# Performance work log

Measured on AMD Instinct MI355X. Metric: run time of the kernel, lower is better.

The kernel has to match this reference:

```python
import jax, jax.numpy as jnp
import numpy as np

EPS = 1e-5
GROUPS = 4


def _bn(x, g, b, axes):
    # training-mode batch norm (fresh torch module runs in train mode): biased var
    mean = x.mean(axes, keepdims=True)
    var = x.var(axes, keepdims=True)
    sh = (1, -1) + (1,) * (x.ndim - 2)
    return (x - mean) * jax.lax.rsqrt(var + EPS) * g.reshape(sh) + b.reshape(sh)


def _prelu(x, a):
    return jnp.where(x >= 0, x, a * x)


def _avgpool2(x):
    B, C, H, W = x.shape
    return x.reshape(B, C, H // 2, 2, W // 2, 2).mean(axis=(3, 5))


def _axial(x, dim, qkv_w, qkv_g, qkv_b, sim_g, sim_b, rel_emb, out_g, out_b):
    # x: [B, C, H, W]; dim==0 attends over H, dim==1 over W
    if dim == 0:
        x = jnp.transpose(x, (0, 3, 1, 2))  # [B, W, C, H]
    else:
        x = jnp.transpose(x, (0, 2, 1, 3))  # [B, H, C, W]
    B, D1, C, A = x.shape
    x = x.reshape(B * D1, C, A)
    # 1x1 conv1d (no bias) + BN1d
    qkv = jnp.einsum('oc,nca->noa', qkv_w, x)
    qkv = _bn(qkv, qkv_g, qkv_b, axes=(0, 2))
    gc = qkv.shape[1] // GROUPS // 2  # group_channels
    qkv = qkv.reshape(B * D1, GROUPS, 2 * gc, A)
    q = qkv[:, :, : gc // 2]
    k = qkv[:, :, gc // 2: gc]
    v = qkv[:, :, gc:]
    # relative position embeddings gathered into [2*gc, A, A]
    ri = jnp.arange(A)[:, None] - jnp.arange(A)[None, :] + A - 1  # [A, A]
    emb = rel_emb[:, ri]
    qe, ke, ve = emb[: gc // 2], emb[gc // 2: gc], emb[gc:]
    q_emb = jnp.einsum('ngci,cij->ngij', q, qe)
    k_emb = jnp.einsum('ngci,cij->ngij', k, ke)
    qk = jnp.einsum('ngci,ngcj->ngij', q_emb, k_emb)
    sim = jnp.concatenate([qk, q_emb, k_emb], axis=1)  # [N, 3g, A, A]
    sim = _bn(sim, sim_g, sim_b, axes=(0, 2, 3))
    sim = sim.reshape(B * D1, 3, GROUPS, A, A).sum(axis=1)
    sim = jax.nn.softmax(sim, axis=3)
    am = jnp.einsum('ngij,ngcj->ngci', sim, v)
    ame = jnp.einsum('ngij,cij->ngci', sim, ve)
    # cat along last dim then view -> equivalent to stacking pairs on a new axis
    out = jnp.stack([am, ame], axis=3).reshape(B * D1, 2 * GROUPS * gc, A)
    out = _bn(out, out_g, out_b, axes=(0, 2))
    out = out.reshape(B, D1, GROUPS * gc, 2, A).sum(axis=3)
    if dim == 0:
        return jnp.transpose(out, (0, 2, 3, 1))  # [B, C_out, H, W]
    return jnp.transpose(out, (0, 2, 1, 3))


def _cbn(x, g, b, lin_w, latent):
    x = _bn(x, g, b, axes=(0, 2, 3))
    sb = lin_w @ latent  # [2*C]
    C = x.shape[1]
    scale, bias = sb[:C], sb[C:]
    return scale[None, :, None, None] * x + bias[None, :, None, None]


def _forward(input, latent_vector, w_in, cbn1_g, cbn1_b, cbn1_lin, prelu1,
             ax0_qkv_w, ax0_qkv_g, ax0_qkv_b, ax0_sim_g, ax0_sim_b, ax0_rel_emb, ax0_out_g, ax0_out_b,
             ax1_qkv_w, ax1_qkv_g, ax1_qkv_b, ax1_sim_g, ax1_sim_b, ax1_rel_emb, ax1_out_g, ax1_out_b,
             w_out, cbn2_g, cbn2_b, cbn2_lin, prelu2):
    out = jnp.einsum('oc,bchw->bohw', w_in, input)
    out = _prelu(_cbn(out, cbn1_g, cbn1_b, cbn1_lin, latent_vector), prelu1)
    out = _axial(out, 0, ax0_qkv_w, ax0_qkv_g, ax0_qkv_b, ax0_sim_g, ax0_sim_b, ax0_rel_emb, ax0_out_g, ax0_out_b)
    out = _axial(out, 1, ax1_qkv_w, ax1_qkv_g, ax1_qkv_b, ax1_sim_g, ax1_sim_b, ax1_rel_emb, ax1_out_g, ax1_out_b)
    out = _avgpool2(out)
    out = jnp.einsum('oc,bchw->bohw', w_out, out)
    out = _cbn(out, cbn2_g, cbn2_b, cbn2_lin, latent_vector)
    out = out + _avgpool2(input)  # residual_mapping is Identity (in==out channels)
    return _prelu(out, prelu2)


def setup_inputs() -> dict:
    key = jax.random.key(0)
    ks = jax.random.split(key, 12)
    C, L, S = 64, 256, 128
    gc = C // GROUPS  # 16
    d = {}
    d['input'] = jax.random.normal(ks[0], (4, C, S, S), dtype=jnp.float32)
    d['latent_vector'] = jax.random.normal(ks[1], (L,), dtype=jnp.float32)
    d['w_in'] = jax.random.normal(ks[2], (C, C), dtype=jnp.float32) * 0.1
    d['cbn1_g'] = jnp.ones((C,), jnp.float32)
    d['cbn1_b'] = jnp.zeros((C,), jnp.float32)
    d['cbn1_lin'] = jax.random.normal(ks[3], (2 * C, L), dtype=jnp.float32) * 0.05
    d['prelu1'] = jnp.float32(0.25)
    for i, k1, k2 in [(0, ks[4], ks[5]), (1, ks[6], ks[7])]:
        d[f'ax{i}_qkv_w'] = jax.random.normal(k1, (2 * C, C), dtype=jnp.float32) * 0.1
        d[f'ax{i}_qkv_g'] = jnp.ones((2 * C,), jnp.float32)
        d[f'ax{i}_qkv_b'] = jnp.zeros((2 * C,), jnp.float32)
        d[f'ax{i}_sim_g'] = jnp.ones((3 * GROUPS,), jnp.float32)
        d[f'ax{i}_sim_b'] = jnp.zeros((3 * GROUPS,), jnp.float32)
        d[f'ax{i}_rel_emb'] = jax.random.normal(k2, (2 * gc, 2 * S - 1), dtype=jnp.float32)
        d[f'ax{i}_out_g'] = jnp.ones((2 * C,), jnp.float32)
        d[f'ax{i}_out_b'] = jnp.zeros((2 * C,), jnp.float32)
    d['w_out'] = jax.random.normal(ks[8], (C, C), dtype=jnp.float32) * 0.1
    d['cbn2_g'] = jnp.ones((C,), jnp.float32)
    d['cbn2_b'] = jnp.zeros((C,), jnp.float32)
    d['cbn2_lin'] = jax.random.normal(ks[9], (2 * C, L), dtype=jnp.float32) * 0.05
    d['prelu2'] = jnp.float32(0.25)
    return d


def reference(input, latent_vector, w_in, cbn1_g, cbn1_b, cbn1_lin, prelu1,
              ax0_qkv_w, ax0_qkv_g, ax0_qkv_b, ax0_sim_g, ax0_sim_b, ax0_rel_emb, ax0_out_g, ax0_out_b,
              ax1_qkv_w, ax1_qkv_g, ax1_qkv_b, ax1_sim_g, ax1_sim_b, ax1_rel_emb, ax1_out_g, ax1_out_b,
              w_out, cbn2_g, cbn2_b, cbn2_lin, prelu2):
    return _forward(input, latent_vector, w_in, cbn1_g, cbn1_b, cbn1_lin, prelu1,
                    ax0_qkv_w, ax0_qkv_g, ax0_qkv_b, ax0_sim_g, ax0_sim_b, ax0_rel_emb, ax0_out_g, ax0_out_b,
                    ax1_qkv_w, ax1_qkv_g, ax1_qkv_b, ax1_sim_g, ax1_sim_b, ax1_rel_emb, ax1_out_g, ax1_out_b,
                    w_out, cbn2_g, cbn2_b, cbn2_lin, prelu2)
```

## Files before the change

kernel.cpp:

```cpp
#include <hip/hip_runtime.h>

#define EPS 1e-5f
#define SP 16
#define SWA(x) ((((x) >> 2) & 3) << 3)

typedef __attribute__((ext_vector_type(4))) _Float16 h4;
typedef __attribute__((ext_vector_type(8))) _Float16 h8;
typedef __attribute__((ext_vector_type(4))) float f4;
typedef __attribute__((ext_vector_type(4))) unsigned int u4;

#define WS_SB1        0
#define WS_SB2        128
#define WS_STAT_C1    256
#define WS_STAT_QKV0  2304
#define WS_STAT_QKV1  6400
#define WS_STAT_SIM0  10496
#define WS_STAT_SIM1  10880
#define WS_STAT_OUT0  11264
#define WS_STAT_OUT1  15360
#define WS_STAT_C2    19456
#define WS_STAT_END   21504
#define WS_COEFQ0     21504
#define WS_COEFQ1     21760

#define WS_R1  32768
#define WS_R2  (WS_R1 + 8388608)
#define WS_R3  (WS_R2 + 8388608)

#define SIM_CNT_INV (1.f / 1048576.f)

#define L_QEA 0
#define L_KEB 32768
#define L_RET 65536
#define L_AQ  73728
#define L_AK  77824
#define L_V   73728

__device__ __forceinline__ float wred(float v) {
    #pragma unroll
    for (int off = 32; off > 0; off >>= 1) v += __shfl_down(v, off, 64);
    return v;
}

__global__ void k_prep0(const float* __restrict__ lin1, const float* __restrict__ lin2,
                        const float* __restrict__ latent, float* __restrict__ ws) {
    int t = threadIdx.x;
    for (int i = 256 + t; i < WS_STAT_END; i += 256) ws[i] = 0.f;
    const float* lin = (t < 128) ? lin1 : lin2;
    int row = t & 127;
    float s = 0.f;
    for (int l = 0; l < 256; ++l) s += lin[row * 256 + l] * latent[l];
    ws[(t < 128 ? WS_SB1 : WS_SB2) + row] = s;
}

__global__ __launch_bounds__(256) void k_conv1(const float* __restrict__ in,
                                               const float* __restrict__ w,
                                               float* __restrict__ out,
                                               float* __restrict__ stat) {
    __shared__ float ws_[2048];
    __shared__ float sred[2][4][32];
    int t = threadIdx.x;
    int lane = t & 63, wv = t >> 6;
    int oh = blockIdx.x & 1;
    int pb = blockIdx.x >> 1;
    for (int i = t; i < 2048; i += 256) ws_[i] = w[oh * 2048 + i];
    __syncthreads();
    int p  = pb * 256 + t;
    int b  = p >> 14, hw = p & 16383;
    const float* ip = in + b * 64 * 16384 + hw;
    float x[64];
    #pragma unroll
    for (int c = 0; c < 64; ++c) x[c] = ip[c * 16384];
    float* op = out + b * 64 * 16384 + hw + oh * 32 * 16384;
    for (int o2 = 0; o2 < 32; ++o2) {
        float acc = 0.f;
        #pragma unroll
        for (int c = 0; c < 64; ++c) acc += ws_[o2 * 64 + c] * x[c];
        op[o2 * 16384] = acc;
        float s = wred(acc), ss = wred(acc * acc);
        if (lane == 0) { sred[0][wv][o2] = s; sred[1][wv][o2] = ss; }
    }
    __syncthreads();
    if (t < 64) {
        int o2 = t & 31, st = t >> 5;
        float v = sred[st][0][o2] + sred[st][1][o2] + sred[st][2][o2] + sred[st][3][o2];
        atomicAdd(&stat[(st * 64 + oh * 32 + o2) * SP], v);
    }
}

__global__ __launch_bounds__(256) void k_t1t(const float* __restrict__ src, float* __restrict__ dst,
                                             const float* __restrict__ ws,
                                             const float* __restrict__ g1,
                                             const float* __restrict__ b1,
                                             const float* __restrict__ prelu1) {
    __shared__ float tile[32][33];
    int bid = blockIdx.x;
    int wt = bid & 3, ht = (bid >> 2) & 3, c = (bid >> 4) & 63, b = bid >> 10;
    float mean = ws[WS_STAT_C1 + c * SP] * (1.f / 65536.f);
    float var  = ws[WS_STAT_C1 + (64 + c) * SP] * (1.f / 65536.f) - mean * mean;
    float ab = g1[c] * rsqrtf(var + EPS);
    float sc = ws[WS_SB1 + c], bi = ws[WS_SB1 + 64 + c];
    float A = sc * ab;
    float Bb = sc * (b1[c] - mean * ab) + bi;
    float slope = *prelu1;
    int tx = threadIdx.x & 31, ty = threadIdx.x >> 5;
    const float* sp = src + ((b * 64 + c) * 128 + ht * 32) * 128 + wt * 32;
    for (int r = 0; r < 4; ++r) {
        float v = sp[(ty + r * 8) * 128 + tx];
        v = A * v + Bb;
        v = v >= 0.f ? v : slope * v;
        tile[ty + r * 8][tx] = v;
    }
    __syncthreads();
    float* dp = dst + b * 1048576 + (wt * 32) * 8192 + c * 128 + ht * 32;
    for (int r = 0; r < 4; ++r)
        dp[(ty + r * 8) * 8192 + tx] = tile[tx][ty + r * 8];
}

__global__ __launch_bounds__(256) void k_qkvm(const float* __restrict__ x, const float* __restrict__ w,
                                              _Float16* __restrict__ out, float* __restrict__ statq,
                                              int SB, int SR, int SC) {
    __shared__ __align__(16) _Float16 Wh[8192];
    __shared__ __align__(16) _Float16 Xt[8192];
    int t = threadIdx.x;
    int lane = t & 63, wv = t >> 6;
    int l15 = lane & 15, g4 = lane >> 4;
    int n = (blockIdx.x & 7) * 64 + (blockIdx.x >> 3);
    int b = n >> 7, r = n & 127;
    for (int i = t; i < 8192; i += 256) {
        int o = i >> 6, c = i & 63;
        Wh[o * 64 + (c ^ ((o & 7) << 3))] = (_Float16)w[i];
    }
    const float* xp = x + b * SB + r * SR;
    for (int i = t; i < 8192; i += 256) {
        int c = i >> 7, a = i & 127;
        Xt[a * 64 + (c ^ ((a & 7) << 3))] = (_Float16)xp[c * SC + a];
    }
    __syncthreads();
    _Float16* op = out + n * 16384;
    float sA[2][4] = {{0.f,0.f,0.f,0.f},{0.f,0.f,0.f,0.f}};
    float qA[2][4] = {{0.f,0.f,0.f,0.f},{0.f,0.f,0.f,0.f}};
    #pragma unroll
    for (int ot2 = 0; ot2 < 2; ++ot2) {
        int orow = (wv * 2 + ot2) * 16 + l15;
        h8 af[2];
        #pragma unroll
        for (int kk = 0; kk < 2; ++kk)
            af[kk] = *(const h8*)&Wh[orow * 64 + ((kk * 32 + g4 * 8) ^ ((orow & 7) << 3))];
        #pragma unroll
        for (int at = 0; at < 8; ++at) {
            int arow = at * 16 + l15;
            f4 c4 = {0.f, 0.f, 0.f, 0.f};
            #pragma unroll
            for (int kk = 0; kk < 2; ++kk) {
                h8 bf = *(const h8*)&Xt[arow * 64 + ((kk * 32 + g4 * 8) ^ ((arow & 7) << 3))];
                c4 = __builtin_amdgcn_mfma_f32_16x16x32_f16(af[kk], bf, c4, 0, 0, 0);
            }
            #pragma unroll
            for (int r4 = 0; r4 < 4; ++r4) {
                int o = (wv * 2 + ot2) * 16 + g4 * 4 + r4;
                float v = c4[r4];
                op[o * 128 + at * 16 + l15] = (_Float16)v;
                sA[ot2][r4] += v; qA[ot2][r4] += v * v;
            }
        }
    }
    #pragma unroll
    for (int ot2 = 0; ot2 < 2; ++ot2)
        #pragma unroll
        for (int r4 = 0; r4 < 4; ++r4) {
            float s = sA[ot2][r4], ss = qA[ot2][r4];
            #pragma unroll
            for (int msk = 1; msk < 16; msk <<= 1) {
                s += __shfl_xor(s, msk, 64); ss += __shfl_xor(ss, msk, 64);
            }
            if (l15 == 0) {
                int o = (wv * 2 + ot2) * 16 + g4 * 4 + r4;
                atomicAdd(&statq[o * SP], s);
                atomicAdd(&statq[(128 + o) * SP], ss);
            }
        }
}

__global__ void k_coefq(const float* __restrict__ statq, const float* __restrict__ qg,
                        const float* __restrict__ qb, float* __restrict__ cq) {
    int c = threadIdx.x; if (c >= 128) return;
    float mean = statq[c * SP] * (1.f / 65536.f);
    float var  = statq[(128 + c) * SP] * (1.f / 65536.f) - mean * mean;
    float A = qg[c] * rsqrtf(var + EPS);
    cq[c] = A;
    cq[128 + c] = qb[c] - mean * A;
}

__device__ __forceinline__ void stage_aqk(unsigned char* L, const _Float16* qkv,
                                          const float* cq, int n, int g, int t) {
    const _Float16* qp = qkv + n * 16384 + g * 32 * 128;
    #pragma unroll
    for (int k = 0; k < 4; ++k) {
        int i = t + k * 512;
        int a = i & 127, cc = i >> 7;
        int ch = g * 32 + cc;
        float v = cq[ch] * (float)qp[cc * 128 + a] + cq[128 + ch];
        _Float16 h = (_Float16)v;
        int off = a * 32 + ((cc * 2) ^ SWA(a));
        *(_Float16*)(L + L_AQ + off) = (cc < 8) ? h : (_Float16)0.f;
        *(_Float16*)(L + L_AK + off) = (cc < 8) ? (_Float16)0.f : h;
    }
}

__device__ __forceinline__ void stage_ret(unsigned char* L, const float* remb, int crow0, int t) {
    #pragma unroll
    for (int k = 0; k < 8; ++k) {
        int i = t + k * 512;
        int d = i & 255, c = i >> 8;
        float v = (d < 255) ? remb[(crow0 + c) * 255 + d] : 0.f;
        *(_Float16*)(L + L_RET + d * 32 + ((c * 2) ^ SWA(d))) = (_Float16)v;
    }
}

template <bool STATS>
__device__ __forceinline__ void build_emb(unsigned char* L, int w, int l15, int g4, float* s) {
    int at = w;
    int arow = at * 16 + l15;
    int aoff = arow * 32 + ((g4 * 8) ^ SWA(arow));
    h4 aq = *(const h4*)(L + L_AQ + aoff);
    h4 ak = *(const h4*)(L + L_AK + aoff);
    int abase = at * 16 + g4 * 4;
    #pragma unroll
    for (int m = 0; m < 9; ++m) {
        int drow = (at + m) * 16 + l15;
        h4 bf = *(const h4*)(L + L_RET + drow * 32 + ((g4 * 8) ^ SWA(drow)));
        f4 z = {0.f, 0.f, 0.f, 0.f};
        f4 dq = __builtin_amdgcn_mfma_f32_16x16x16f16(aq, bf, z, 0, 0, 0);
        f4 dk = __builtin_amdgcn_mfma_f32_16x16x16f16(ak, bf, z, 0, 0, 0);
        #pragma unroll
        for (int r = 0; r < 4; ++r) {
            int a = abase + r;
            int b = 127 + a - drow;
            bool ok = (m == 0 || m == 8) ? (b >= 0 && b < 128) : true;
            if (ok) {
                int off = b * 256 + ((a * 2) ^ ((b & 7) << 4));
                *(_Float16*)(L + L_QEA + off) = (_Float16)dq[r];
                *(_Float16*)(L + L_KEB + off) = (_Float16)dk[r];
                if (STATS) {
                    s[0] += dq[r]; s[1] += dq[r] * dq[r];
                    s[2] += dk[r]; s[3] += dk[r] * dk[r];
                }
            }
        }
    }
}

__device__ __forceinline__ void qk_mfma(unsigned char* L, int i0, int l15, int g4, f4 acc[8]) {
    h8 af[4];
    #pragma unroll
    for (int ks = 0; ks < 4; ++ks) {
        int row = i0 + l15;
        af[ks] = *(const h8*)(L + L_QEA + row * 256 + ((ks * 64 + g4 * 16) ^ ((row & 7) << 4)));
    }
    #pragma unroll
    for (int tj = 0; tj < 8; ++tj) {
        h8 bf[4];
        #pragma unroll
        for (int ks = 0; ks < 4; ++ks) {
            int row = tj * 16 + l15;
            bf[ks] = *(const h8*)(L + L_KEB + row * 256 + ((ks * 64 + g4 * 16) ^ ((row & 7) << 4)));
        }
        f4 c = {0.f, 0.f, 0.f, 0.f};
        #pragma unroll
        for (int ks = 0; ks < 4; ++ks)
            c = __builtin_amdgcn_mfma_f32_16x16x32_f16(af[ks], bf[ks], c, 0, 0, 0);
        acc[tj] = c;
    }
}

__global__ __launch_bounds__(512, 4) void k_passA(const _Float16* __restrict__ qkv,
                                                  const float* __restrict__ remb,
                                                  const float* __restrict__ cq,
                                                  float* __restrict__ statsim) {
    __shared__ __align__(16) unsigned char L[81920];
    int t = threadIdx.x;
    int lane = t & 63, w = t >> 6;
    int l15 = lane & 15, g4 = lane >> 4;
    int ts = (blockIdx.x & 7) * 32 + (blockIdx.x >> 3);
    int n = (ts >> 2) * 8, g = ts & 3;

    stage_aqk(L, qkv, cq, n, g, t);
    stage_ret(L, remb, 0, t);
    __syncthreads();

    float es[4] = {0.f, 0.f, 0.f, 0.f};
    build_emb<true>(L, w, l15, g4, es);
    __syncthreads();

    float* red = (float*)(L + L_AK);
    #pragma unroll
    for (int k = 0; k < 4; ++k) es[k] = wred(es[k]);
    if (lane == 0) {
        red[w * 4 + 0] = es[0]; red[w * 4 + 1] = es[1];
        red[w * 4 + 2] = es[2]; red[w * 4 + 3] = es[3];
    }

    f4 acc[8];
    qk_mfma(L, w * 16, l15, g4, acc);

    float s = 0.f, ss = 0.f;
    #pragma unroll
    for (int tj = 0; tj < 8; ++tj)
        #pragma unroll
        for (int r = 0; r < 4; ++r) { float x = acc[tj][r]; s += x; ss += x * x; }
    s = wred(s); ss = wred(ss);
    if (lane == 0) { red[32 + w * 2] = s; red[33 + w * 2] = ss; }
    __syncthreads();

    if (t < 6) {
        float v = 0.f;
        int dst;
        if (t == 0)      { for (int k = 0; k < 8; ++k) v += red[32 + 2 * k]; dst = g; }
        else if (t == 1) { for (int k = 0; k < 8; ++k) v += red[33 + 2 * k]; dst = 12 + g; }
        else if (t == 2) { for (int k = 0; k < 8; ++k) v += red[k * 4 + 0];  dst = 4 + g; }
        else if (t == 3) { for (int k = 0; k < 8; ++k) v += red[k * 4 + 1];  dst = 16 + g; }
        else if (t == 4) { for (int k = 0; k < 8; ++k) v += red[k * 4 + 2];  dst = 8 + g; }
        else             { for (int k = 0; k < 8; ++k) v += red[k * 4 + 3];  dst = 20 + g; }
        atomicAdd(&statsim[dst * SP], v);
    }
}

__global__ __launch_bounds__(512, 4) void k_passB(const _Float16* __restrict__ qkv,
                                                  const float* __restrict__ remb,
                                                  const float* __restrict__ cq,
                                                  const float* __restrict__ statsim,
                                                  const float* __restrict__ simg,
                                                  const float* __restrict__ simb,
                                                  unsigned int* __restrict__ att2,
                                                  float* __restrict__ statout) {
    __shared__ __align__(16) unsigned char L[81920];
    int t = threadIdx.x;
    int lane = t & 63, w = t >> 6;
    int l15 = lane & 15, g4 = lane >> 4;
    int s0 = (blockIdx.x & 7) * 256 + (blockIdx.x >> 3);
    int n = s0 >> 2, g = s0 & 3;

    stage_aqk(L, qkv, cq, n, g, t);
    stage_ret(L, remb, 0, t);
    __syncthreads();

    build_emb<false>(L, w, l15, g4, nullptr);
    __syncthreads();

    #pragma unroll
    for (int k = 0; k < 4; ++k) {
        int i = t + k * 512;
        int j = i & 127, c = i >> 7;
        int ch = g * 32 + 16 + c;
        float v = cq[ch] * (float)qkv[n * 16384 + ch * 128 + j] + cq[128 + ch];
        *(_Float16*)(L + L_V + c * 256 + ((j * 2) ^ ((c & 7) << 4))) = (_Float16)v;
    }
    #pragma unroll
    for (int k = 0; k < 8; ++k) {
        int i = t + k * 512;
        int d = i & 255, c = i >> 8;
        float v = (d < 255) ? remb[(16 + c) * 255 + d] : 0.f;
        *(_Float16*)(L + L_RET + c * 512 + ((d * 2) ^ ((c & 7) << 4))) = (_Float16)v;
    }

    int i0 = w * 16;
    f4 acc[8];
    qk_mfma(L, i0, l15, g4, acc);

    float Aqk, Aqe, Ake, Cst = 0.f;
    {
        float A3[3];
        #pragma unroll
        for (int k = 0; k < 3; ++k) {
            int ch = k * 4 + g;
            float mean = statsim[ch * SP] * SIM_CNT_INV;
            float var  = statsim[(12 + ch) * SP] * SIM_CNT_INV - mean * mean;
            float A = simg[ch] * rsqrtf(var + EPS);
            A3[k] = A;
            Cst += simb[ch] - mean * A;
        }
        Aqk = A3[0]; Aqe = A3[1]; Ake = A3[2];
    }
    int ib = (i0 + g4 * 4) * 2;
    #pragma unroll
    for (int tj = 0; tj < 8; ++tj) {
        int j = tj * 16 + l15;
        h4 q4 = *(const h4*)(L + L_QEA + j * 256 + (ib ^ ((j & 7) << 4)));
        h4 k4 = *(const h4*)(L + L_KEB + j * 256 + (ib ^ ((j & 7) << 4)));
        #pragma unroll
        for (int r = 0; r < 4; ++r)
            acc[tj][r] = Aqk * acc[tj][r] + Aqe * (float)q4[r] + Ake * (float)k4[r] + Cst;
    }

    float inv4[4];
    #pragma unroll
    for (int r = 0; r < 4; ++r) {
        float m = acc[0][r];
        #pragma unroll
        for (int tj = 1; tj < 8; ++tj) m = fmaxf(m, acc[tj][r]);
        #pragma unroll
        for (int msk = 1; msk < 16; msk <<= 1) m = fmaxf(m, __shfl_xor(m, msk, 64));
        float s = 0.f;
        #pragma unroll
        for (int tj = 0; tj < 8; ++tj) {
            float e = __expf(acc[tj][r] - m);
            acc[tj][r] = e; s += e;
        }
        #pragma unroll
        for (int msk = 1; msk < 16; msk <<= 1) s += __shfl_xor(s, msk, 64);
        inv4[r] = 1.f / s;
    }

    _Float16 ph[4][8];
    #pragma unroll
    for (int r = 0; r < 4; ++r)
        #pragma unroll
        for (int tj = 0; tj < 8; ++tj)
            ph[r][tj] = (_Float16)(acc[tj][r] * inv4[r]);
    __syncthreads();

    int lo = w >> 1;
    int lo2 = (w >> 2) << 1;

    #pragma unroll
    for (int r = 0; r < 4; ++r) {
        int i = i0 + g4 * 4 + r;
        int swz = (i & 7) << 4;
        #pragma unroll
        for (int tj = 0; tj < 8; ++tj) {
            int j = tj * 16 + l15;
            *(_Float16*)(L + L_QEA + i * 256 + ((j * 2) ^ swz)) = ph[r][tj];
        }
    }
    if (w >= 4) {
        #pragma unroll
        for (int u = 0; u < 6; ++u) {
            u4 zz = {0u, 0u, 0u, 0u};
            *(u4*)(L + w * 8192 + (lane >> 2) * 512 + lo2 * 64 + ((u * 4 + (lane & 3)) << 4)) = zz;
        }
        #pragma unroll
        for (int r = 0; r < 4; ++r) {
            int i = i0 + g4 * 4 + r;
            int swz = (i & 7) << 4;
            #pragma unroll
            for (int tj = 0; tj < 8; ++tj) {
                int j = tj * 16 + l15;
                int d = 127 + i - j;
                *(_Float16*)(L + i * 512 + ((d * 2) ^ swz)) = ph[r][tj];
            }
        }
    }

    h8 vf[4];
    #pragma unroll
    for (int ks = 0; ks < 4; ++ks)
        vf[ks] = *(const h8*)(L + L_V + l15 * 256 + ((ks * 64 + g4 * 16) ^ ((l15 & 7) << 4)));
    int row = i0 + l15;
    int sw = (row & 7) << 4;
    f4 cam = {0.f, 0.f, 0.f, 0.f};
    #pragma unroll
    for (int ks = 0; ks < 4; ++ks) {
        h8 pf = *(const h8*)(L + L_QEA + row * 256 + ((ks * 64 + g4 * 16) ^ sw));
        cam = __builtin_amdgcn_mfma_f32_16x16x32_f16(vf[ks], pf, cam, 0, 0, 0);
    }
    __syncthreads();

    if (w < 4) {
        #pragma unroll
        for (int u = 0; u < 6; ++u) {
            u4 zz = {0u, 0u, 0u, 0u};
            *(u4*)(L + w * 8192 + (lane >> 2) * 512 + lo2 * 64 + ((u * 4 + (lane & 3)) << 4)) = zz;
        }
        #pragma unroll
        for (int r = 0; r < 4; ++r) {
            int i = i0 + g4 * 4 + r;
            int swz = (i & 7) << 4;
            #pragma unroll
            for (int tj = 0; tj < 8; ++tj) {
                int j = tj * 16 + l15;
                int d = 127 + i - j;
                *(_Float16*)(L + i * 512 + ((d * 2) ^ swz)) = ph[r][tj];
            }
        }
    }

    h8 vef[5];
    #pragma unroll
    for (int u = 0; u < 5; ++u) {
        int ks = lo + u;
        vef[u] = *(const h8*)(L + L_RET + l15 * 512 + ((ks * 64 + g4 * 16) ^ ((l15 & 7) << 4)));
    }
    f4 cae = {0.f, 0.f, 0.f, 0.f};
    #pragma unroll
    for (int u = 0; u < 5; ++u) {
        int ks = lo + u;
        h8 phf = *(const h8*)(L + row * 512 + ((ks * 64 + g4 * 16) ^ sw));
        cae = __builtin_amdgcn_mfma_f32_16x16x32_f16(vef[u], phf, cae, 0, 0, 0);
    }

    unsigned int* attL = (unsigned int*)(L + L_V);
    int i = i0 + l15;
    #pragma unroll
    for (int r = 0; r < 4; ++r) {
        union { _Float16 h[2]; unsigned int u; } pk;
        pk.h[0] = (_Float16)cam[r];
        pk.h[1] = (_Float16)cae[r];
        attL[(g4 * 4 + r) * 128 + i] = pk.u;
    }

    float* sredW = (float*)(L + w * 8192);
    #pragma unroll
    for (int r = 0; r < 4; ++r) {
        float sa = cam[r], qa = cam[r] * cam[r];
        float se = cae[r], qe = cae[r] * cae[r];
        #pragma unroll
        for (int msk = 1; msk < 16; msk <<= 1) {
            sa += __shfl_xor(sa, msk, 64); qa += __shfl_xor(qa, msk, 64);
            se += __shfl_xor(se, msk, 64); qe += __shfl_xor(qe, msk, 64);
        }
        if (l15 == 0) {
            int base = g4 * 16 + r * 4;
            sredW[base + 0] = sa; sredW[base + 1] = qa;
            sredW[base + 2] = se; sredW[base + 3] = qe;
        }
    }
    __syncthreads();

    unsigned int* ab = att2 + n * 8192 + g * 2048;
    *(u4*)(ab + t * 4) = *(const u4*)(attL + t * 4);

    if (t < 64) {
        int lc = t & 31, stat = t >> 5;
        int c = lc >> 1, s = lc & 1;
        int gg4 = c >> 2, r = c & 3;
        float v = 0.f;
        #pragma unroll
        for (int ww = 0; ww < 8; ++ww)
            v += ((const float*)L)[ww * 2048 + gg4 * 16 + r * 4 + 2 * s + stat];
        atomicAdd(&statout[(stat * 128 + g * 32 + lc) * SP], v);
    }
}

__global__ __launch_bounds__(256) void k_finish0(const unsigned int* __restrict__ att2,
                                                 const float* __restrict__ statout,
                                                 const float* __restrict__ og,
                                                 const float* __restrict__ ob,
                                                 float* __restrict__ t2) {
    __shared__ float tile[8][32][33];
    __shared__ float cf[256];
    int t = threadIdx.x;
    if (t < 128) {
        float mean = statout[t * SP] * (1.f / 65536.f);
        float var  = statout[(128 + t) * SP] * (1.f / 65536.f) - mean * mean;
        float A = og[t] * rsqrtf(var + EPS);
        cf[t] = A;
        cf[128 + t] = ob[t] - mean * A;
    }
    __syncthreads();
    int bid = blockIdx.x;
    int wt = bid & 3, ht = (bid >> 2) & 3, cg = (bid >> 4) & 7, b = bid >> 7;
    for (int i = t; i < 8192; i += 256) {
        int h = i & 31, w = (i >> 5) & 31, cl = i >> 10;
        int c_out = cg * 8 + cl;
        int chg = (c_out >> 4) * 32 + (c_out & 15) * 2;
        int p = chg >> 1;
        union { unsigned int u; _Float16 h2[2]; } pk;
        pk.u = att2[((b * 128 + wt * 32 + w) * 64 + p) * 128 + ht * 32 + h];
        tile[cl][w][h] = cf[chg] * (float)pk.h2[0] + cf[128 + chg]
                       + cf[chg + 1] * (float)pk.h2[1] + cf[129 + chg];
    }
    __syncthreads();
    for (int i = t; i < 8192; i += 256) {
        int w = i & 31, h = (i >> 5) & 31, cl = i >> 10;
        t2[((b * 64 + cg * 8 + cl) * 128 + ht * 32 + h) * 128 + wt * 32 + w] = tile[cl][w][h];
    }
}

__global__ __launch_bounds__(64) void k_conv2f(const unsigned int* __restrict__ att2,
                                               const float* __restrict__ statout,
                                               const float* __restrict__ og,
                                               const float* __restrict__ ob,
                                               const float* __restrict__ w,
                                               float* __restrict__ out,
                                               float* __restrict__ statc2) {
    __shared__ float ws_[4096];
    __shared__ float cf[4][64];
    __shared__ float otile[64][65];
    int t = threadIdx.x;
    for (int i = t; i < 4096; i += 64) ws_[i] = w[i];
    {
        int chg = (t >> 4) * 32 + (t & 15) * 2;
        float m0 = statout[chg * SP] * (1.f / 65536.f);
        float v0 = statout[(128 + chg) * SP] * (1.f / 65536.f) - m0 * m0;
        float A0 = og[chg] * rsqrtf(v0 + EPS);
        cf[0][t] = A0; cf[1][t] = ob[chg] - m0 * A0;
        float m1 = statout[(chg + 1) * SP] * (1.f / 65536.f);
        float v1 = statout[(129 + chg) * SP] * (1.f / 65536.f) - m1 * m1;
        float A1 = og[chg + 1] * rsqrtf(v1 + EPS);
        cf[2][t] = A1; cf[3][t] = ob[chg + 1] - m1 * A1;
    }
    __syncthreads();
    int p = blockIdx.x * 64 + t;
    int b = p >> 12, yx = p & 4095, y = yx >> 6, x = yx & 63;
    const unsigned int* ap = att2 + (b * 128 + 2 * y) * 8192 + 2 * x;
    float xc[64];
    #pragma unroll
    for (int c = 0; c < 64; ++c) {
        int pp = (c >> 4) * 16 + (c & 15);
        const unsigned int* q = ap + pp * 128;
        union { unsigned int u; _Float16 h2[2]; } a0, a1, a2, a3;
        a0.u = q[0]; a1.u = q[1]; a2.u = q[8192]; a3.u = q[8193];
        float s0 = (float)a0.h2[0] + (float)a1.h2[0] + (float)a2.h2[0] + (float)a3.h2[0];
        float s1 = (float)a0.h2[1] + (float)a1.h2[1] + (float)a2.h2[1] + (float)a3.h2[1];
        xc[c] = 0.25f * (cf[0][c] * s0 + cf[2][c] * s1) + cf[1][c] + cf[3][c];
    }
    float* op = out + b * 262144 + yx;
    for (int o = 0; o < 64; ++o) {
        float acc = 0.f;
        #pragma unroll
        for (int c = 0; c < 64; ++c) acc += ws_[o * 64 + c] * xc[c];
        op[o * 4096] = acc;
        otile[o][t] = acc;
    }
    __syncthreads();
    float s = 0.f, ss = 0.f;
    #pragma unroll
    for (int k = 0; k < 64; ++k) { float v = otile[t][k]; s += v; ss += v * v; }
    atomicAdd(&statc2[t * SP], s);
    atomicAdd(&statc2[(64 + t) * SP], ss);
}

__global__ __launch_bounds__(256) void k_final(const float* __restrict__ c2out,
                                               const float* __restrict__ input,
                                               const float* __restrict__ ws,
                                               const float* __restrict__ g2,
                                               const float* __restrict__ b2,
                                               const float* __restrict__ prelu2,
                                               float* __restrict__ out) {
    int q = blockIdx.x * 256 + threadIdx.x;
    int x4 = (q & 15) << 2, y = (q >> 4) & 63, o = (q >> 10) & 63, b = q >> 16;
    float mean = ws[WS_STAT_C2 + o * SP] * (1.f / 16384.f);
    float var  = ws[WS_STAT_C2 + (64 + o) * SP] * (1.f / 16384.f) - mean * mean;
    float ab = g2[o] * rsqrtf(var + EPS);
    float sc = ws[WS_SB2 + o], bi = ws[WS_SB2 + 64 + o];
    float A = sc * ab;
    float B = sc * (b2[o] - mean * ab) + bi;
    float slope = *prelu2;
    int base = ((b * 64 + o) * 64 + y) * 64 + x4;
    float4 c = *(const float4*)&c2out[base];
    const float* ip = input + ((b * 64 + o) * 128 + 2 * y) * 128 + 2 * x4;
    float4 r0a = *(const float4*)&ip[0];
    float4 r0b = *(const float4*)&ip[4];
    float4 r1a = *(const float4*)&ip[128];
    float4 r1b = *(const float4*)&ip[132];
    float4 r;
    float v0 = A * c.x + B + 0.25f * (r0a.x + r0a.y + r1a.x + r1a.y);
    float v1 = A * c.y + B + 0.25f * (r0a.z + r0a.w + r1a.z + r1a.w);
    float v2 = A * c.z + B + 0.25f * (r0b.x + r0b.y + r1b.x + r1b.y);
    float v3 = A * c.w + B + 0.25f * (r0b.z + r0b.w + r1b.z + r1b.w);
    r.x = v0 >= 0.f ? v0 : slope * v0;
    r.y = v1 >= 0.f ? v1 : slope * v1;
    r.z = v2 >= 0.f ? v2 : slope * v2;
    r.w = v3 >= 0.f ? v3 : slope * v3;
    *(float4*)&out[base] = r;
}

extern "C" void kernel_launch(void* const* d_in, const int* in_sizes, int n_in,
                              void* d_out, int out_size, void* d_ws, size_t ws_size,
                              hipStream_t stream) {
    const float* input    = (const float*)d_in[0];
    const float* latent   = (const float*)d_in[1];
    const float* w_in     = (const float*)d_in[2];
    const float* cbn1_g   = (const float*)d_in[3];
    const float* cbn1_b   = (const float*)d_in[4];
    const float* cbn1_lin = (const float*)d_in[5];
    const float* prelu1   = (const float*)d_in[6];
    const float* ax_qkv_w[2] = {(const float*)d_in[7],  (const float*)d_in[15]};
    const float* ax_qkv_g[2] = {(const float*)d_in[8],  (const float*)d_in[16]};
    const float* ax_qkv_b[2] = {(const float*)d_in[9],  (const float*)d_in[17]};
    const float* ax_sim_g[2] = {(const float*)d_in[10], (const float*)d_in[18]};
    const float* ax_sim_b[2] = {(const float*)d_in[11], (const float*)d_in[19]};
    const float* ax_rel[2]   = {(const float*)d_in[12], (const float*)d_in[20]};
    const float* ax_out_g[2] = {(const float*)d_in[13], (const float*)d_in[21]};
    const float* ax_out_b[2] = {(const float*)d_in[14], (const float*)d_in[22]};
    const float* w_out    = (const float*)d_in[23];
    const float* cbn2_g   = (const float*)d_in[24];
    const float* cbn2_b   = (const float*)d_in[25];
    const float* cbn2_lin = (const float*)d_in[26];
    const float* prelu2   = (const float*)d_in[27];

    float* ws    = (float*)d_ws;
    float* out0  = ws + WS_R1;
    float* t1t   = ws + WS_R1 + 4194304;
    unsigned int* att2 = (unsigned int*)(ws + WS_R1);
    _Float16* qkvh = (_Float16*)(ws + WS_R2);
    float* t23   = ws + WS_R3;
    float* c2o   = ws + WS_R3;
    float* dst   = (float*)d_out;

    k_prep0<<<1, 256, 0, stream>>>(cbn1_lin, cbn2_lin, latent, ws);
    k_conv1<<<512, 256, 0, stream>>>(input, w_in, out0, ws + WS_STAT_C1);
    k_t1t<<<4096, 256, 0, stream>>>(out0, t1t, ws, cbn1_g, cbn1_b, prelu1);

    k_qkvm<<<512, 256, 0, stream>>>(t1t, ax_qkv_w[0], qkvh, ws + WS_STAT_QKV0,
                                    1048576, 8192, 128);
    k_coefq<<<1, 128, 0, stream>>>(ws + WS_STAT_QKV0, ax_qkv_g[0], ax_qkv_b[0], ws + WS_COEFQ0);
    k_passA<<<256, 512, 0, stream>>>(qkvh, ax_rel[0], ws + WS_COEFQ0, ws + WS_STAT_SIM0);
    k_passB<<<2048, 512, 0, stream>>>(qkvh, ax_rel[0], ws + WS_COEFQ0, ws + WS_STAT_SIM0,
                                      ax_sim_g[0], ax_sim_b[0], att2, ws + WS_STAT_OUT0);
    k_finish0<<<512, 256, 0, stream>>>(att2, ws + WS_STAT_OUT0, ax_out_g[0], ax_out_b[0], t23);

    k_qkvm<<<512, 256, 0, stream>>>(t23, ax_qkv_w[1], qkvh, ws + WS_STAT_QKV1,
                                    1048576, 128, 16384);
    k_coefq<<<1, 128, 0, stream>>>(ws + WS_STAT_QKV1, ax_qkv_g[1], ax_qkv_b[1], ws + WS_COEFQ1);
    k_passA<<<256, 512, 0, stream>>>(qkvh, ax_rel[1], ws + WS_COEFQ1, ws + WS_STAT_SIM1);
    k_passB<<<2048, 512, 0, stream>>>(qkvh, ax_rel[1], ws + WS_COEFQ1, ws + WS_STAT_SIM1,
                                      ax_sim_g[1], ax_sim_b[1], att2, ws + WS_STAT_OUT1);

    k_conv2f<<<256, 64, 0, stream>>>(att2, ws + WS_STAT_OUT1, ax_out_g[1], ax_out_b[1],
                                     w_out, c2o, ws + WS_STAT_C2);
    k_final<<<1024, 256, 0, stream>>>(c2o, input, ws, cbn2_g, cbn2_b, prelu2, dst);
}
```

Baseline: 324.5 us.

## Widen conv2f to four waves per block and prioritize MFMA in passB

The final 1x1 conv kernel moves from one 64-thread wave per block to four waves. The block first stages the pooled, BN-normalized activations into shared memory with coalesced loads, then each wave computes 16 output channels, and the BN stats are reduced with wave reductions before the atomics. This targets low occupancy and the large per-thread register array in the old conv kernel. Separately, passB raises wave priority around its QK MFMA section. The cost is an extra shared tile and more atomics per block.

Result: faster. 308.0 us (-5.1%).

```diff
diff --git a/kernel.cpp b/kernel.cpp
--- a/kernel.cpp
+++ b/kernel.cpp
@@ -366,7 +366,9 @@
 
     int i0 = w * 16;
     f4 acc[8];
+    __builtin_amdgcn_s_setprio(1);
     qk_mfma(L, i0, l15, g4, acc);
+    __builtin_amdgcn_s_setprio(0);
 
     float Aqk, Aqe, Ake, Cst = 0.f;
     {
@@ -577,19 +579,20 @@
     }
 }
 
-__global__ __launch_bounds__(64) void k_conv2f(const unsigned int* __restrict__ att2,
-                                               const float* __restrict__ statout,
-                                               const float* __restrict__ og,
-                                               const float* __restrict__ ob,
-                                               const float* __restrict__ w,
-                                               float* __restrict__ out,
-                                               float* __restrict__ statc2) {
+__global__ __launch_bounds__(256) void k_conv2f(const unsigned int* __restrict__ att2,
+                                                const float* __restrict__ statout,
+                                                const float* __restrict__ og,
+                                                const float* __restrict__ ob,
+                                                const float* __restrict__ w,
+                                                float* __restrict__ out,
+                                                float* __restrict__ statc2) {
     __shared__ float ws_[4096];
     __shared__ float cf[4][64];
-    __shared__ float otile[64][65];
+    __shared__ float xcs[64][64];
     int t = threadIdx.x;
-    for (int i = t; i < 4096; i += 64) ws_[i] = w[i];
-    {
+    int lane = t & 63, wv = t >> 6;
+    for (int i = t; i < 4096; i += 256) ws_[i] = w[i];
+    if (t < 64) {
         int chg = (t >> 4) * 32 + (t & 15) * 2;
         float m0 = statout[chg * SP] * (1.f / 65536.f);
         float v0 = statout[(128 + chg) * SP] * (1.f / 65536.f) - m0 * m0;
@@ -601,34 +604,43 @@
         cf[2][t] = A1; cf[3][t] = ob[chg + 1] - m1 * A1;
     }
     __syncthreads();
-    int p = blockIdx.x * 64 + t;
-    int b = p >> 12, yx = p & 4095, y = yx >> 6, x = yx & 63;
-    const unsigned int* ap = att2 + (b * 128 + 2 * y) * 8192 + 2 * x;
-    float xc[64];
-    #pragma unroll
-    for (int c = 0; c < 64; ++c) {
-        int pp = (c >> 4) * 16 + (c & 15);
-        const unsigned int* q = ap + pp * 128;
+    int p0 = blockIdx.x * 64;
+    int b = p0 >> 12;
+    int y = (p0 & 4095) >> 6;
+    const unsigned int* aprow = att2 + (b * 128 + 2 * y) * 8192;
+    #pragma unroll
+    for (int k = 0; k < 16; ++k) {
+        int e = t + k * 256;
+        int px = e & 63, c = e >> 6;
+        const unsigned int* q = aprow + c * 128 + 2 * px;
         union { unsigned int u; _Float16 h2[2]; } a0, a1, a2, a3;
         a0.u = q[0]; a1.u = q[1]; a2.u = q[8192]; a3.u = q[8193];
         float s0 = (float)a0.h2[0] + (float)a1.h2[0] + (float)a2.h2[0] + (float)a3.h2[0];
         float s1 = (float)a0.h2[1] + (float)a1.h2[1] + (float)a2.h2[1] + (float)a3.h2[1];
-        xc[c] = 0.25f * (cf[0][c] * s0 + cf[2][c] * s1) + cf[1][c] + cf[3][c];
-    }
-    float* op = out + b * 262144 + yx;
-    for (int o = 0; o < 64; ++o) {
-        float acc = 0.f;
-        #pragma unroll
-        for (int c = 0; c < 64; ++c) acc += ws_[o * 64 + c] * xc[c];
-        op[o * 4096] = acc;
-        otile[o][t] = acc;
-    }
-    __syncthreads();
-    float s = 0.f, ss = 0.f;
-    #pragma unroll
-    for (int k = 0; k < 64; ++k) { float v = otile[t][k]; s += v; ss += v * v; }
-    atomicAdd(&statc2[t * SP], s);
-    atomicAdd(&statc2[(64 + t) * SP], ss);
+        xcs[c][px] = 0.25f * (cf[0][c] * s0 + cf[2][c] * s1) + cf[1][c] + cf[3][c];
+    }
+    __syncthreads();
+    int yx = (p0 + lane) & 4095;
+    float acc[16];
+    #pragma unroll
+    for (int u = 0; u < 16; ++u) acc[u] = 0.f;
+    for (int c = 0; c < 64; ++c) {
+        float xv = xcs[c][lane];
+        #pragma unroll
+        for (int u = 0; u < 16; ++u)
+            acc[u] += ws_[(wv * 16 + u) * 64 + c] * xv;
+    }
+    float* ob_ = out + b * 262144 + yx;
+    #pragma unroll
+    for (int u = 0; u < 16; ++u) {
+        int o = wv * 16 + u;
+        ob_[o * 4096] = acc[u];
+        float s = wred(acc[u]), ss = wred(acc[u] * acc[u]);
+        if (lane == 0) {
+            atomicAdd(&statc2[o * SP], s);
+            atomicAdd(&statc2[(64 + o) * SP], ss);
+        }
+    }
 }
 
 __global__ __launch_bounds__(256) void k_final(const float* __restrict__ c2out,
@@ -718,7 +730,7 @@
     k_passB<<<2048, 512, 0, stream>>>(qkvh, ax_rel[1], ws + WS_COEFQ1, ws + WS_STAT_SIM1,
                                       ax_sim_g[1], ax_sim_b[1], att2, ws + WS_STAT_OUT1);
 
-    k_conv2f<<<256, 64, 0, stream>>>(att2, ws + WS_STAT_OUT1, ax_out_g[1], ax_out_b[1],
-                                     w_out, c2o, ws + WS_STAT_C2);
+    k_conv2f<<<256, 256, 0, stream>>>(att2, ws + WS_STAT_OUT1, ax_out_g[1], ax_out_b[1],
+                                      w_out, c2o, ws + WS_STAT_C2);
     k_final<<<1024, 256, 0, stream>>>(c2o, input, ws, cbn2_g, cbn2_b, prelu2, dst);
 }
```
